# Kernel tuning notes

Measured on AMD Instinct MI355X. Metric: run time of the kernel, lower is better.

## Reference

```python
import jax, jax.numpy as jnp
import numpy as np

IN_DIM = 64

def setup_inputs() -> dict:
    key = jax.random.key(0)
    ks = jax.random.split(key, 9)
    B, C, H, W = 4, IN_DIM, 256, 256
    scale = 1.0 / np.sqrt(3 * C)  # conv fan-in init scale
    return {
        'rgb': jax.random.normal(ks[0], (B, C, H, W), dtype=jnp.float32),
        'hsv': jax.random.normal(ks[1], (B, C, H, W), dtype=jnp.float32),
        'lab': jax.random.normal(ks[2], (B, C, H, W), dtype=jnp.float32),
        'Wq': jax.random.normal(ks[3], (C, 3 * C), dtype=jnp.float32) * scale,
        'bq': jax.random.normal(ks[4], (C,), dtype=jnp.float32) * scale,
        'Wk': jax.random.normal(ks[5], (C, 3 * C), dtype=jnp.float32) * scale,
        'bk': jax.random.normal(ks[6], (C,), dtype=jnp.float32) * scale,
        'Wv': jax.random.normal(ks[7], (C, 3 * C), dtype=jnp.float32) * scale,
        'bv': jax.random.normal(ks[8], (C,), dtype=jnp.float32) * scale,
    }

def _proj(x, W, b):
    # 1x1 conv: [B,3C,H,W] x [C,3C] -> [B,C,H,W]
    return jnp.einsum('oc,bchw->bohw', W, x) + b[None, :, None, None]

def reference(rgb, hsv, lab, Wq, bq, Wk, bk, Wv, bv):
    B, C, H, W = rgb.shape
    combined = jnp.concatenate([rgb, hsv, lab], axis=1)  # [B,3C,H,W]
    q = _proj(combined, Wq, bq).reshape(B, C, H * W)     # [B,C,N]
    k = _proj(combined, Wk, bk).reshape(B, C, H * W)     # [B,C,N]
    v = _proj(combined, Wv, bv).reshape(B, C, H * W)     # [B,C,N]
    energy = jnp.einsum('bcn,bdn->bcd', q, k) * (C ** -0.5)  # [B,C,C]
    attention = jax.nn.softmax(energy, axis=-1)
    out = jnp.einsum('bcd,bdn->bcn', attention, v)           # [B,C,N]
    return out.reshape(B, C, H, W)
```

## Files before the change

### kernel.cpp

```cpp
#include <hip/hip_runtime.h>
#include <cstddef>


#define NPIX 65536

typedef _Float16 half4_t __attribute__((ext_vector_type(4)));
typedef _Float16 half8_t __attribute__((ext_vector_type(8)));
typedef float f32x4_t __attribute__((ext_vector_type(4)));

__global__ void k0_zero(float* __restrict__ p, int n) {
  int i = blockIdx.x * 256 + threadIdx.x;
  if (i < n) p[i] = 0.0f;
}

__global__ __launch_bounds__(512) void k1_gram(
    const float* __restrict__ rgb, const float* __restrict__ hsv, const float* __restrict__ lab,
    float* __restrict__ G, float* __restrict__ S, float* __restrict__ part, int mode) {
  __shared__ alignas(16) _Float16 ldsb[2][6144];
  float* slds = (float*)&ldsb[0][0];

  const int t = threadIdx.x;
  const int lane = t & 63;
  const int w = t >> 6;
  const int wi = w >> 2;
  const int wj = w & 3;
  const int b = blockIdx.y;
  const int bx = blockIdx.x;
  const int n0 = bx * 512;

  const int rr = t >> 3;
  const int c8 = t & 7;
  const float* gp0 = rgb + (size_t)(b * 64 + rr) * NPIX + n0 + 4 * c8;
  const float* gp1 = hsv + (size_t)(b * 64 + rr) * NPIX + n0 + 4 * c8;
  const float* gp2 = lab + (size_t)(b * 64 + rr) * NPIX + n0 + 4 * c8;

  const int swz = (rr >> 1) & 3;
  const int wbase = ((c8 >> 1) ^ swz) * 8 + (c8 & 1) * 4;
  const int wof0 = (0 * 64 + rr) * 32 + wbase;
  const int wof1 = (1 * 64 + rr) * 32 + wbase;
  const int wof2 = (2 * 64 + rr) * 32 + wbase;

  f32x4_t acc[6][3];
  const f32x4_t zero4 = {0.0f, 0.0f, 0.0f, 0.0f};
#pragma unroll
  for (int a = 0; a < 6; ++a)
#pragma unroll
    for (int j = 0; j < 3; ++j) acc[a][j] = zero4;
  float sr0 = 0.f, sr1 = 0.f, sr2 = 0.f;

  float4 R0, R1, R2;
  auto loadR = [&](int cc) {
    R0 = *(const float4*)(gp0 + cc * 32);
    R1 = *(const float4*)(gp1 + cc * 32);
    R2 = *(const float4*)(gp2 + cc * 32);
  };
  auto writeL = [&](int par) {
    _Float16* buf = &ldsb[par][0];
    half4_t h;
    sr0 += (R0.x + R0.y) + (R0.z + R0.w);
    h.x = (_Float16)R0.x; h.y = (_Float16)R0.y; h.z = (_Float16)R0.z; h.w = (_Float16)R0.w;
    *(half4_t*)(buf + wof0) = h;
    sr1 += (R1.x + R1.y) + (R1.z + R1.w);
    h.x = (_Float16)R1.x; h.y = (_Float16)R1.y; h.z = (_Float16)R1.z; h.w = (_Float16)R1.w;
    *(half4_t*)(buf + wof1) = h;
    sr2 += (R2.x + R2.y) + (R2.z + R2.w);
    h.x = (_Float16)R2.x; h.y = (_Float16)R2.y; h.z = (_Float16)R2.z; h.w = (_Float16)R2.w;
    *(half4_t*)(buf + wof2) = h;
  };

  const int l15 = lane & 15;
  const int g = lane >> 4;
  auto compute = [&](int par) {
    const _Float16* buf = &ldsb[par][0];
    half8_t fB[3];
#pragma unroll
    for (int j = 0; j < 3; ++j) {
      int rB = (wj * 3 + j) * 16 + l15;
      fB[j] = *(const half8_t*)(buf + rB * 32 + ((g ^ ((rB >> 1) & 3)) << 3));
    }
#pragma unroll
    for (int a = 0; a < 6; ++a) {
      int rA = (wi * 6 + a) * 16 + l15;
      half8_t fa = *(const half8_t*)(buf + rA * 32 + ((g ^ ((rA >> 1) & 3)) << 3));
#pragma unroll
      for (int j = 0; j < 3; ++j)
        acc[a][j] = __builtin_amdgcn_mfma_f32_16x16x32_f16(fa, fB[j], acc[a][j], 0, 0, 0);
    }
  };

  loadR(0);
  for (int cc = 0; cc < 16; ++cc) {
    writeL(cc & 1);
    asm volatile("s_waitcnt lgkmcnt(0)" ::: "memory");
    __builtin_amdgcn_sched_barrier(0);
    __builtin_amdgcn_s_barrier();
    if (cc + 1 < 16) loadR(cc + 1);
    compute(cc & 1);
  }

  if (mode == 2) {
    float* pb = part + (size_t)(b * 128 + bx) * 37056;
#pragma unroll
    for (int a = 0; a < 6; ++a)
#pragma unroll
      for (int j = 0; j < 3; ++j) {
        int tt = (wi * 6 + a) * 12 + (wj * 3 + j);
        *(f32x4_t*)(pb + tt * 256 + lane * 4) = acc[a][j];
      }
  } else {
    float* Gb = G + b * 36864;
#pragma unroll
    for (int a = 0; a < 6; ++a)
#pragma unroll
      for (int j = 0; j < 3; ++j) {
#pragma unroll
        for (int r = 0; r < 4; ++r) {
          int gr = (wi * 6 + a) * 16 + ((lane >> 4) << 2) + r;
          int gc = (wj * 3 + j) * 16 + (lane & 15);
          atomicAdd(Gb + gr * 192 + gc, acc[a][j][r]);
        }
      }
  }

  slds[(0 * 64 + rr) * 8 + c8] = sr0;
  slds[(1 * 64 + rr) * 8 + c8] = sr1;
  slds[(2 * 64 + rr) * 8 + c8] = sr2;
  __syncthreads();
  if (t < 192) {
    float v = 0.f;
#pragma unroll
    for (int q = 0; q < 8; ++q) v += slds[t * 8 + q];
    if (mode == 2)
      part[(size_t)(b * 128 + bx) * 37056 + 36864 + t] = v;
    else
      atomicAdd(S + b * 192 + t, v);
  }
}

__global__ void k1r_reduce(const float* __restrict__ part, float* __restrict__ G,
                           float* __restrict__ S, int P) {
  int idx = blockIdx.x * 256 + threadIdx.x;
  if (idx >= 4 * 37056) return;
  int b = idx / 37056;
  int flat = idx % 37056;
  const float* base = part + (size_t)b * P * 37056 + flat;
  float v0 = 0.f, v1 = 0.f, v2 = 0.f, v3 = 0.f;
  for (int q = 0; q < P; q += 4) {
    v0 += base[(size_t)(q + 0) * 37056];
    v1 += base[(size_t)(q + 1) * 37056];
    v2 += base[(size_t)(q + 2) * 37056];
    v3 += base[(size_t)(q + 3) * 37056];
  }
  float v = (v0 + v1) + (v2 + v3);
  if (flat < 36864) {
    int tt = flat >> 8;
    int I = tt / 12, J = tt % 12;
    int r = flat & 255;
    int lane = r >> 2, rg = r & 3;
    int row = I * 16 + ((lane >> 4) << 2) + rg;
    int col = J * 16 + (lane & 15);
    G[b * 36864 + row * 192 + col] = v;
  } else {
    S[b * 192 + (flat - 36864)] = v;
  }
}

__global__ __launch_bounds__(256) void k2_small(
    const float* __restrict__ G, const float* __restrict__ S,
    const float* __restrict__ Wq, const float* __restrict__ bq,
    const float* __restrict__ Wk, const float* __restrict__ bk,
    const float* __restrict__ Wv, const float* __restrict__ bv,
    _Float16* __restrict__ Mh, float* __restrict__ c0w) {
  const int b = blockIdx.y;
  const int cbase = blockIdx.x * 8;
  const int t = threadIdx.x;
  __shared__ float T1[192 * 9];
  __shared__ float el[64 * 8];
  __shared__ float sq[8];
  __shared__ float sk[64];
  const float* Gb = G + b * 36864;
  const float* Sb = S + b * 192;

  if (t < 8) {
    float a = 0.f;
    const float* wq = Wq + (cbase + t) * 192;
    for (int i = 0; i < 192; ++i) a = fmaf(wq[i], Sb[i], a);
    sq[t] = a;
  } else if (t < 72) {
    int d = t - 8;
    float a = 0.f;
    const float* wk = Wk + d * 192;
    for (int j = 0; j < 192; ++j) a = fmaf(wk[j], Sb[j], a);
    sk[d] = a;
  }
  for (int e = t; e < 1536; e += 256) {
    int j = e % 192, cp = e / 192;
    const float* wq = Wq + (cbase + cp) * 192;
    float a = 0.f;
    for (int i = 0; i < 192; ++i) a = fmaf(wq[i], Gb[i * 192 + j], a);
    T1[j * 9 + cp] = a;
  }
  __syncthreads();
  for (int e = t; e < 512; e += 256) {
    int cp = e & 7, d = e >> 3;
    const float* wk = Wk + d * 192;
    float a = 0.f;
    for (int j = 0; j < 192; ++j) a = fmaf(T1[j * 9 + cp], wk[j], a);
    float bqc = bq[cbase + cp], bkd = bk[d];
    a += bqc * sk[d] + bkd * sq[cp] + 65536.0f * bqc * bkd;
    el[d * 8 + cp] = a * 0.125f;
  }
  __syncthreads();
  if (t < 8) {
    float mx = -3.0e38f;
    for (int d = 0; d < 64; ++d) mx = fmaxf(mx, el[d * 8 + t]);
    float sum = 0.f;
    for (int d = 0; d < 64; ++d) {
      float pv = expf(el[d * 8 + t] - mx);
      el[d * 8 + t] = pv;
      sum += pv;
    }
    float inv = 1.0f / sum;
    for (int d = 0; d < 64; ++d) el[d * 8 + t] *= inv;
  }
  __syncthreads();
  for (int e = t; e < 1536; e += 256) {
    int i = e % 192, cp = e / 192;
    int c = cbase + cp;
    float a = 0.f;
    for (int d = 0; d < 64; ++d) a = fmaf(el[d * 8 + cp], Wv[d * 192 + i], a);
    Mh[(size_t)b * 12288 + c * 192 + (i ^ ((c & 7) << 3))] = (_Float16)a;
  }
  if (t < 8) {
    float a = 0.f;
    for (int d = 0; d < 64; ++d) a = fmaf(el[d * 8 + t], bv[d], a);
    c0w[b * 64 + cbase + t] = a;
  }
}

__global__ __launch_bounds__(256, 3) void k3_out(
    const float* __restrict__ rgb, const float* __restrict__ hsv, const float* __restrict__ lab,
    const _Float16* __restrict__ Mh, const float* __restrict__ c0w, float* __restrict__ out) {
  __shared__ alignas(16) _Float16 lds_m[12288];
  __shared__ alignas(16) _Float16 lds_x[8192];
  __shared__ float c0l[64];
  const int t = threadIdx.x;
  const int lane = t & 63;
  const int w = t >> 6;
  const int b = blockIdx.y;
  const int nblk = blockIdx.x * 256;

  {
    const float4* msrc = (const float4*)(Mh + (size_t)b * 12288);
    float4* mdst = (float4*)lds_m;
#pragma unroll
    for (int k = 0; k < 6; ++k) mdst[t + 256 * k] = msrc[t + 256 * k];
    if (t < 64) c0l[t] = c0w[b * 64 + t];
  }

  const int xi = t & 31;
  const int ng = t >> 5;
  const float* srcs[3] = {rgb, hsv, lab};

  f32x4_t acc[4][4];
  const f32x4_t zero4 = {0.0f, 0.0f, 0.0f, 0.0f};
#pragma unroll
  for (int i = 0; i < 4; ++i)
#pragma unroll
    for (int j = 0; j < 4; ++j) acc[i][j] = zero4;

  float4 xr[8];
  auto xload = [&](int kc) {
    int ig = kc * 32 + xi;
    const float* p = srcs[ig >> 6] + (size_t)(b * 64 + (ig & 63)) * NPIX + nblk + ng * 32;
#pragma unroll
    for (int f = 0; f < 8; ++f) xr[f] = *(const float4*)(p + f * 4);
  };
  auto xwrite = [&]() {
#pragma unroll
    for (int f = 0; f < 8; ++f) {
      int n = ng * 32 + f * 4;
      lds_x[(n + 0) * 32 + (xi ^ 0)]  = (_Float16)xr[f].x;
      lds_x[(n + 1) * 32 + (xi ^ 8)]  = (_Float16)xr[f].y;
      lds_x[(n + 2) * 32 + (xi ^ 16)] = (_Float16)xr[f].z;
      lds_x[(n + 3) * 32 + (xi ^ 24)] = (_Float16)xr[f].w;
    }
  };

  const int g = lane >> 4;
  const int l15 = lane & 15;

  xload(0);
  for (int kc = 0; kc < 6; ++kc) {
    xwrite();
    __syncthreads();
    if (kc + 1 < 6) xload(kc + 1);
    half8_t fx[4], fm[4];
#pragma unroll
    for (int nt = 0; nt < 4; ++nt) {
      int n = w * 64 + nt * 16 + l15;
      fx[nt] = *(const half8_t*)(lds_x + n * 32 + ((8 * g) ^ ((n & 3) << 3)));
    }
#pragma unroll
    for (int ct = 0; ct < 4; ++ct) {
      int c = ct * 16 + l15;
      fm[ct] = *(const half8_t*)(lds_m + c * 192 + ((kc * 32 + 8 * g) ^ ((c & 7) << 3)));
    }
#pragma unroll
    for (int nt = 0; nt < 4; ++nt)
#pragma unroll
      for (int ct = 0; ct < 4; ++ct)
        acc[nt][ct] = __builtin_amdgcn_mfma_f32_16x16x32_f16(fx[nt], fm[ct], acc[nt][ct], 0, 0, 0);
    __syncthreads();
  }

#pragma unroll
  for (int ct = 0; ct < 4; ++ct) {
    int c = ct * 16 + l15;
    float c0v = c0l[c];
#pragma unroll
    for (int nt = 0; nt < 4; ++nt) {
      int n = nblk + w * 64 + nt * 16 + 4 * g;
      float4 o;
      o.x = acc[nt][ct][0] + c0v;
      o.y = acc[nt][ct][1] + c0v;
      o.z = acc[nt][ct][2] + c0v;
      o.w = acc[nt][ct][3] + c0v;
      *(float4*)(out + (size_t)(b * 64 + c) * NPIX + n) = o;
    }
  }
}

extern "C" void kernel_launch(void* const* d_in, const int* in_sizes, int n_in,
                              void* d_out, int out_size, void* d_ws, size_t ws_size,
                              hipStream_t stream) {
  const float* rgb = (const float*)d_in[0];
  const float* hsv = (const float*)d_in[1];
  const float* lab = (const float*)d_in[2];
  const float* Wq = (const float*)d_in[3];
  const float* bq = (const float*)d_in[4];
  const float* Wk = (const float*)d_in[5];
  const float* bk = (const float*)d_in[6];
  const float* Wv = (const float*)d_in[7];
  const float* bv = (const float*)d_in[8];
  float* out = (float*)d_out;
  float* ws = (float*)d_ws;

  float* G = ws;
  float* S = ws + 147456;
  _Float16* Mh = (_Float16*)(ws + 148224);
  float* c0w = ws + 172800;
  float* part = ws + 173056;
  const size_t need2 = (size_t)(173056 + 512 * 37056) * 4;
  const int mode = ws_size >= need2 ? 2 : 0;

  if (mode == 0)
    k0_zero<<<dim3(579), dim3(256), 0, stream>>>(ws, 148224);

  k1_gram<<<dim3(128, 4), dim3(512), 0, stream>>>(rgb, hsv, lab, G, S, part, mode);
  if (mode)
    k1r_reduce<<<dim3(579), dim3(256), 0, stream>>>(part, G, S, 128);
  k2_small<<<dim3(8, 4), dim3(256), 0, stream>>>(G, S, Wq, bq, Wk, bk, Wv, bv, Mh, c0w);
  k3_out<<<dim3(256, 4), dim3(256), 0, stream>>>(rgb, hsv, lab, Mh, c0w, out);
}
```

Baseline: 167.0 us.

## Compute only upper-triangular Gram tiles and mirror to fill symmetric half

The Gram kernel now computes only the 78 upper-triangular 16x16 tiles of the symmetric 192x192 matrix instead of all 144, spreading them over 8 waves. This roughly halves the MFMA work and the partial-sum traffic written and reduced. The reduce kernel writes each value to both mirrored positions, and a new mirror kernel fills the lower half in atomic mode. It also drops the double-buffered LDS in favour of a single buffer with two barriers per step, which may expose more load latency.

```diff
diff --git a/kernel.cpp b/kernel.cpp
--- a/kernel.cpp
+++ b/kernel.cpp
@@ -8,161 +8,225 @@
 typedef _Float16 half8_t __attribute__((ext_vector_type(8)));
 typedef float f32x4_t __attribute__((ext_vector_type(4)));
 
+constexpr int TRI_I[78] = {
+  0,0,0,0,0,0,0,0,0,0,0,0,
+  1,1,1,1,1,1,1,1,1,1,1,
+  2,2,2,2,2,2,2,2,2,2,
+  3,3,3,3,3,3,3,3,3,
+  4,4,4,4,4,4,4,4,
+  5,5,5,5,5,5,5,
+  6,6,6,6,6,6,
+  7,7,7,7,7,
+  8,8,8,8,
+  9,9,9,
+  10,10,
+  11};
+constexpr int TRI_J[78] = {
+  0,1,2,3,4,5,6,7,8,9,10,11,
+  1,2,3,4,5,6,7,8,9,10,11,
+  2,3,4,5,6,7,8,9,10,11,
+  3,4,5,6,7,8,9,10,11,
+  4,5,6,7,8,9,10,11,
+  5,6,7,8,9,10,11,
+  6,7,8,9,10,11,
+  7,8,9,10,11,
+  8,9,10,11,
+  9,10,11,
+  10,11,
+  11};
+
+#define PSZ 20160
+
 __global__ void k0_zero(float* __restrict__ p, int n) {
   int i = blockIdx.x * 256 + threadIdx.x;
   if (i < n) p[i] = 0.0f;
 }
 
+template <int BASE, int CNT>
+__device__ __forceinline__ void mfma_run(const _Float16* __restrict__ buf,
+                                         f32x4_t* __restrict__ acc, int l15, int g) {
+  half8_t fA;
+#pragma unroll
+  for (int tt = 0; tt < CNT; ++tt) {
+    const int t = BASE + tt;
+    if (tt == 0 || TRI_I[t] != TRI_I[t - 1]) {
+      int rA = TRI_I[t] * 16 + l15;
+      fA = *(const half8_t*)(buf + rA * 32 + ((g ^ ((rA >> 1) & 3)) << 3));
+    }
+    int rB = TRI_J[t] * 16 + l15;
+    half8_t fB = *(const half8_t*)(buf + rB * 32 + ((g ^ ((rB >> 1) & 3)) << 3));
+    acc[tt] = __builtin_amdgcn_mfma_f32_16x16x32_f16(fA, fB, acc[tt], 0, 0, 0);
+  }
+}
+
+template <int BASE, int CNT>
+__device__ __forceinline__ void flush_part(const f32x4_t* __restrict__ acc,
+                                           float* __restrict__ pb, int lane) {
+#pragma unroll
+  for (int tt = 0; tt < CNT; ++tt)
+    *(f32x4_t*)(pb + (BASE + tt) * 256 + lane * 4) = acc[tt];
+}
+
+template <int BASE, int CNT>
+__device__ __forceinline__ void flush_atomic(const f32x4_t* __restrict__ acc,
+                                             float* __restrict__ Gb, int lane) {
+#pragma unroll
+  for (int tt = 0; tt < CNT; ++tt) {
+    const int t = BASE + tt;
+#pragma unroll
+    for (int r = 0; r < 4; ++r) {
+      int gr = TRI_I[t] * 16 + ((lane >> 4) << 2) + r;
+      int gc = TRI_J[t] * 16 + (lane & 15);
+      atomicAdd(Gb + gr * 192 + gc, acc[tt][r]);
+    }
+  }
+}
+
 __global__ __launch_bounds__(512) void k1_gram(
     const float* __restrict__ rgb, const float* __restrict__ hsv, const float* __restrict__ lab,
     float* __restrict__ G, float* __restrict__ S, float* __restrict__ part, int mode) {
-  __shared__ alignas(16) _Float16 ldsb[2][6144];
-  float* slds = (float*)&ldsb[0][0];
+  __shared__ alignas(16) _Float16 lds[6144];
+  float* slds = (float*)lds;
 
   const int t = threadIdx.x;
   const int lane = t & 63;
   const int w = t >> 6;
-  const int wi = w >> 2;
-  const int wj = w & 3;
   const int b = blockIdx.y;
   const int bx = blockIdx.x;
   const int n0 = bx * 512;
 
-  const int rr = t >> 3;
-  const int c8 = t & 7;
-  const float* gp0 = rgb + (size_t)(b * 64 + rr) * NPIX + n0 + 4 * c8;
-  const float* gp1 = hsv + (size_t)(b * 64 + rr) * NPIX + n0 + 4 * c8;
-  const float* gp2 = lab + (size_t)(b * 64 + rr) * NPIX + n0 + 4 * c8;
-
-  const int swz = (rr >> 1) & 3;
-  const int wbase = ((c8 >> 1) ^ swz) * 8 + (c8 & 1) * 4;
-  const int wof0 = (0 * 64 + rr) * 32 + wbase;
-  const int wof1 = (1 * 64 + rr) * 32 + wbase;
-  const int wof2 = (2 * 64 + rr) * 32 + wbase;
-
-  f32x4_t acc[6][3];
+  const int gq = t & 7;
+  const int r6 = t >> 3;
+  const float* gp0 = rgb + (size_t)(b * 64 + r6) * NPIX + n0 + 4 * gq;
+  const float* gp1 = hsv + (size_t)(b * 64 + r6) * NPIX + n0 + 4 * gq;
+  const float* gp2 = lab + (size_t)(b * 64 + r6) * NPIX + n0 + 4 * gq;
+  const int wsw = (((gq >> 1) ^ ((r6 >> 1) & 3)) << 3) + (gq & 1) * 4;
+  const int wof0 = (0 * 64 + r6) * 32 + wsw;
+  const int wof1 = (1 * 64 + r6) * 32 + wsw;
+  const int wof2 = (2 * 64 + r6) * 32 + wsw;
+
+  f32x4_t acc[10];
   const f32x4_t zero4 = {0.0f, 0.0f, 0.0f, 0.0f};
 #pragma unroll
-  for (int a = 0; a < 6; ++a)
-#pragma unroll
-    for (int j = 0; j < 3; ++j) acc[a][j] = zero4;
+  for (int i = 0; i < 10; ++i) acc[i] = zero4;
   float sr0 = 0.f, sr1 = 0.f, sr2 = 0.f;
 
-  float4 R0, R1, R2;
+  float4 P0, P1, P2;
   auto loadR = [&](int cc) {
-    R0 = *(const float4*)(gp0 + cc * 32);
-    R1 = *(const float4*)(gp1 + cc * 32);
-    R2 = *(const float4*)(gp2 + cc * 32);
+    P0 = *(const float4*)(gp0 + cc * 32);
+    P1 = *(const float4*)(gp1 + cc * 32);
+    P2 = *(const float4*)(gp2 + cc * 32);
   };
-  auto writeL = [&](int par) {
-    _Float16* buf = &ldsb[par][0];
+  auto writeL = [&]() {
     half4_t h;
-    sr0 += (R0.x + R0.y) + (R0.z + R0.w);
-    h.x = (_Float16)R0.x; h.y = (_Float16)R0.y; h.z = (_Float16)R0.z; h.w = (_Float16)R0.w;
-    *(half4_t*)(buf + wof0) = h;
-    sr1 += (R1.x + R1.y) + (R1.z + R1.w);
-    h.x = (_Float16)R1.x; h.y = (_Float16)R1.y; h.z = (_Float16)R1.z; h.w = (_Float16)R1.w;
-    *(half4_t*)(buf + wof1) = h;
-    sr2 += (R2.x + R2.y) + (R2.z + R2.w);
-    h.x = (_Float16)R2.x; h.y = (_Float16)R2.y; h.z = (_Float16)R2.z; h.w = (_Float16)R2.w;
-    *(half4_t*)(buf + wof2) = h;
+    sr0 += (P0.x + P0.y) + (P0.z + P0.w);
+    h.x = (_Float16)P0.x; h.y = (_Float16)P0.y; h.z = (_Float16)P0.z; h.w = (_Float16)P0.w;
+    *(half4_t*)(lds + wof0) = h;
+    sr1 += (P1.x + P1.y) + (P1.z + P1.w);
+    h.x = (_Float16)P1.x; h.y = (_Float16)P1.y; h.z = (_Float16)P1.z; h.w = (_Float16)P1.w;
+    *(half4_t*)(lds + wof1) = h;
+    sr2 += (P2.x + P2.y) + (P2.z + P2.w);
+    h.x = (_Float16)P2.x; h.y = (_Float16)P2.y; h.z = (_Float16)P2.z; h.w = (_Float16)P2.w;
+    *(half4_t*)(lds + wof2) = h;
   };
 
   const int l15 = lane & 15;
   const int g = lane >> 4;
-  auto compute = [&](int par) {
-    const _Float16* buf = &ldsb[par][0];
-    half8_t fB[3];
-#pragma unroll
-    for (int j = 0; j < 3; ++j) {
-      int rB = (wj * 3 + j) * 16 + l15;
-      fB[j] = *(const half8_t*)(buf + rB * 32 + ((g ^ ((rB >> 1) & 3)) << 3));
-    }
-#pragma unroll
-    for (int a = 0; a < 6; ++a) {
-      int rA = (wi * 6 + a) * 16 + l15;
-      half8_t fa = *(const half8_t*)(buf + rA * 32 + ((g ^ ((rA >> 1) & 3)) << 3));
-#pragma unroll
-      for (int j = 0; j < 3; ++j)
-        acc[a][j] = __builtin_amdgcn_mfma_f32_16x16x32_f16(fa, fB[j], acc[a][j], 0, 0, 0);
-    }
-  };
 
   loadR(0);
   for (int cc = 0; cc < 16; ++cc) {
-    writeL(cc & 1);
-    asm volatile("s_waitcnt lgkmcnt(0)" ::: "memory");
-    __builtin_amdgcn_sched_barrier(0);
-    __builtin_amdgcn_s_barrier();
+    writeL();
+    __syncthreads();
     if (cc + 1 < 16) loadR(cc + 1);
-    compute(cc & 1);
-  }
-
-  if (mode == 2) {
-    float* pb = part + (size_t)(b * 128 + bx) * 37056;
-#pragma unroll
-    for (int a = 0; a < 6; ++a)
-#pragma unroll
-      for (int j = 0; j < 3; ++j) {
-        int tt = (wi * 6 + a) * 12 + (wj * 3 + j);
-        *(f32x4_t*)(pb + tt * 256 + lane * 4) = acc[a][j];
-      }
+    switch (w) {
+      case 0: mfma_run<0, 10>(lds, acc, l15, g); break;
+      case 1: mfma_run<10, 10>(lds, acc, l15, g); break;
+      case 2: mfma_run<20, 10>(lds, acc, l15, g); break;
+      case 3: mfma_run<30, 10>(lds, acc, l15, g); break;
+      case 4: mfma_run<40, 10>(lds, acc, l15, g); break;
+      case 5: mfma_run<50, 10>(lds, acc, l15, g); break;
+      case 6: mfma_run<60, 10>(lds, acc, l15, g); break;
+      case 7: mfma_run<70, 8>(lds, acc, l15, g); break;
+    }
+    __syncthreads();
+  }
+
+  if (mode) {
+    float* pb = part + (size_t)(b * 128 + bx) * PSZ;
+    switch (w) {
+      case 0: flush_part<0, 10>(acc, pb, lane); break;
+      case 1: flush_part<10, 10>(acc, pb, lane); break;
+      case 2: flush_part<20, 10>(acc, pb, lane); break;
+      case 3: flush_part<30, 10>(acc, pb, lane); break;
+      case 4: flush_part<40, 10>(acc, pb, lane); break;
+      case 5: flush_part<50, 10>(acc, pb, lane); break;
+      case 6: flush_part<60, 10>(acc, pb, lane); break;
+      case 7: flush_part<70, 8>(acc, pb, lane); break;
+    }
   } else {
     float* Gb = G + b * 36864;
-#pragma unroll
-    for (int a = 0; a < 6; ++a)
-#pragma unroll
-      for (int j = 0; j < 3; ++j) {
-#pragma unroll
-        for (int r = 0; r < 4; ++r) {
-          int gr = (wi * 6 + a) * 16 + ((lane >> 4) << 2) + r;
-          int gc = (wj * 3 + j) * 16 + (lane & 15);
-          atomicAdd(Gb + gr * 192 + gc, acc[a][j][r]);
-        }
-      }
-  }
-
-  slds[(0 * 64 + rr) * 8 + c8] = sr0;
-  slds[(1 * 64 + rr) * 8 + c8] = sr1;
-  slds[(2 * 64 + rr) * 8 + c8] = sr2;
+    switch (w) {
+      case 0: flush_atomic<0, 10>(acc, Gb, lane); break;
+      case 1: flush_atomic<10, 10>(acc, Gb, lane); break;
+      case 2: flush_atomic<20, 10>(acc, Gb, lane); break;
+      case 3: flush_atomic<30, 10>(acc, Gb, lane); break;
+      case 4: flush_atomic<40, 10>(acc, Gb, lane); break;
+      case 5: flush_atomic<50, 10>(acc, Gb, lane); break;
+      case 6: flush_atomic<60, 10>(acc, Gb, lane); break;
+      case 7: flush_atomic<70, 8>(acc, Gb, lane); break;
+    }
+  }
+
+  slds[(0 * 64 + r6) * 8 + gq] = sr0;
+  slds[(1 * 64 + r6) * 8 + gq] = sr1;
+  slds[(2 * 64 + r6) * 8 + gq] = sr2;
   __syncthreads();
   if (t < 192) {
     float v = 0.f;
 #pragma unroll
     for (int q = 0; q < 8; ++q) v += slds[t * 8 + q];
-    if (mode == 2)
-      part[(size_t)(b * 128 + bx) * 37056 + 36864 + t] = v;
+    if (mode)
+      part[(size_t)(b * 128 + bx) * PSZ + 19968 + t] = v;
     else
       atomicAdd(S + b * 192 + t, v);
   }
 }
 
 __global__ void k1r_reduce(const float* __restrict__ part, float* __restrict__ G,
-                           float* __restrict__ S, int P) {
+                           float* __restrict__ S) {
   int idx = blockIdx.x * 256 + threadIdx.x;
-  if (idx >= 4 * 37056) return;
-  int b = idx / 37056;
-  int flat = idx % 37056;
-  const float* base = part + (size_t)b * P * 37056 + flat;
+  if (idx >= 4 * PSZ) return;
+  int b = idx / PSZ;
+  int flat = idx % PSZ;
+  const float* base = part + (size_t)b * 128 * PSZ + flat;
   float v0 = 0.f, v1 = 0.f, v2 = 0.f, v3 = 0.f;
-  for (int q = 0; q < P; q += 4) {
-    v0 += base[(size_t)(q + 0) * 37056];
-    v1 += base[(size_t)(q + 1) * 37056];
-    v2 += base[(size_t)(q + 2) * 37056];
-    v3 += base[(size_t)(q + 3) * 37056];
+#pragma unroll 4
+  for (int q = 0; q < 128; q += 4) {
+    v0 += base[(size_t)(q + 0) * PSZ];
+    v1 += base[(size_t)(q + 1) * PSZ];
+    v2 += base[(size_t)(q + 2) * PSZ];
+    v3 += base[(size_t)(q + 3) * PSZ];
   }
   float v = (v0 + v1) + (v2 + v3);
-  if (flat < 36864) {
+  if (flat < 19968) {
     int tt = flat >> 8;
-    int I = tt / 12, J = tt % 12;
     int r = flat & 255;
     int lane = r >> 2, rg = r & 3;
-    int row = I * 16 + ((lane >> 4) << 2) + rg;
-    int col = J * 16 + (lane & 15);
-    G[b * 36864 + row * 192 + col] = v;
+    int row = TRI_I[tt] * 16 + ((lane >> 4) << 2) + rg;
+    int col = TRI_J[tt] * 16 + (lane & 15);
+    float* Gb = G + b * 36864;
+    Gb[row * 192 + col] = v;
+    Gb[col * 192 + row] = v;
   } else {
-    S[b * 192 + (flat - 36864)] = v;
-  }
+    S[b * 192 + (flat - 19968)] = v;
+  }
+}
+
+__global__ void k1m_mirror(float* __restrict__ G) {
+  int b = blockIdx.y;
+  int idx = blockIdx.x * 256 + threadIdx.x;
+  int i = idx / 192, j = idx % 192;
+  if ((i >> 4) > (j >> 4)) G[b * 36864 + idx] = G[b * 36864 + j * 192 + i];
 }
 
 __global__ __launch_bounds__(256) void k2_small(
@@ -351,15 +415,17 @@
   _Float16* Mh = (_Float16*)(ws + 148224);
   float* c0w = ws + 172800;
   float* part = ws + 173056;
-  const size_t need2 = (size_t)(173056 + 512 * 37056) * 4;
-  const int mode = ws_size >= need2 ? 2 : 0;
-
-  if (mode == 0)
+  const size_t need1 = (size_t)(173056 + 4 * 128 * PSZ) * 4;
+  const int mode = ws_size >= need1 ? 1 : 0;
+
+  if (!mode)
     k0_zero<<<dim3(579), dim3(256), 0, stream>>>(ws, 148224);
 
   k1_gram<<<dim3(128, 4), dim3(512), 0, stream>>>(rgb, hsv, lab, G, S, part, mode);
   if (mode)
-    k1r_reduce<<<dim3(579), dim3(256), 0, stream>>>(part, G, S, 128);
+    k1r_reduce<<<dim3(315), dim3(256), 0, stream>>>(part, G, S);
+  else
+    k1m_mirror<<<dim3(144, 4), dim3(256), 0, stream>>>(G);
   k2_small<<<dim3(8, 4), dim3(256), 0, stream>>>(G, S, Wq, bq, Wk, bk, Wv, bv, Mh, c0w);
   k3_out<<<dim3(256, 4), dim3(256), 0, stream>>>(rgb, hsv, lab, Mh, c0w, out);
 }
```

Measured after the change: 148.4 us (median of 2 runs). 1.13x faster.
